# Kernel optimization log

Hardware: AMD Instinct MI355X
Metric: run time of the kernel (lower is better)

## Reference

```python
import jax, jax.numpy as jnp
import numpy as np

N_NODES = 50000
N_EDGES = 800000
IN_C, HID_C, OUT_C, HEADS = 128, 32, 64, 8
NEG_SLOPE = 0.2


def gat_layer(x, src, dst, W, a_src, a_dst, bias, concat, num_nodes):
    # W: [F_in, H*C]; a_src, a_dst: [H, C]; bias: [H*C] or [C]
    H, C = a_src.shape
    h = (x @ W).reshape(num_nodes, H, C)                      # [N,H,C]
    e_src = (h * a_src).sum(-1)                               # [N,H]
    e_dst = (h * a_dst).sum(-1)                               # [N,H]
    e = jax.nn.leaky_relu(e_src[src] + e_dst[dst], NEG_SLOPE) # [E,H]
    # segment softmax over incoming edges of each destination node
    m = jax.ops.segment_max(e, dst, num_segments=num_nodes)   # [N,H]
    ex = jnp.exp(e - m[dst])
    den = jax.ops.segment_sum(ex, dst, num_segments=num_nodes)
    alpha = ex / (den[dst] + 1e-16)                           # [E,H]
    out = jax.ops.segment_sum(h[src] * alpha[..., None], dst, num_segments=num_nodes)  # [N,H,C]
    out = out.reshape(num_nodes, H * C) if concat else out.mean(axis=1)
    return out + bias


def setup_inputs() -> dict:
    key = jax.random.key(0)
    ks = jax.random.split(key, 10)
    x = jax.random.normal(ks[0], (N_NODES, IN_C), dtype=jnp.float32)
    edge_index = jax.random.randint(ks[1], (2, N_EDGES), 0, N_NODES, dtype=jnp.int64)
    s1 = (2.0 / (IN_C + HID_C * HEADS)) ** 0.5
    s2 = (2.0 / (HID_C * HEADS + OUT_C)) ** 0.5
    return {
        "x": x,
        "edge_index": edge_index,
        "W1": jax.random.normal(ks[2], (IN_C, HEADS * HID_C), dtype=jnp.float32) * s1,
        "a_src1": jax.random.normal(ks[3], (HEADS, HID_C), dtype=jnp.float32) * 0.1,
        "a_dst1": jax.random.normal(ks[4], (HEADS, HID_C), dtype=jnp.float32) * 0.1,
        "b1": jnp.zeros((HEADS * HID_C,), dtype=jnp.float32),
        "W2": jax.random.normal(ks[5], (HEADS * HID_C, OUT_C), dtype=jnp.float32) * s2,
        "a_src2": jax.random.normal(ks[6], (1, OUT_C), dtype=jnp.float32) * 0.1,
        "a_dst2": jax.random.normal(ks[7], (1, OUT_C), dtype=jnp.float32) * 0.1,
        "b2": jnp.zeros((OUT_C,), dtype=jnp.float32),
    }


def reference(x, edge_index, W1, a_src1, a_dst1, b1, W2, a_src2, a_dst2, b2):
    # add self-loops (PyG GATConv default)
    loops = jnp.arange(N_NODES, dtype=edge_index.dtype)
    src = jnp.concatenate([edge_index[0], loops])
    dst = jnp.concatenate([edge_index[1], loops])
    # dropout layers are identity in eval mode
    h = gat_layer(x, src, dst, W1, a_src1, a_dst1, b1, True, N_NODES)
    h = jax.nn.elu(h)
    out = gat_layer(h, src, dst, W2, a_src2, a_dst2, b2, False, N_NODES)
    return out
```

## Files before the change

### kernel.cpp

```cpp
#include <hip/hip_runtime.h>
#include <math.h>

#define N_NODES 50000
#define N_EDGES 800000
#define E_TOT   850000
#define IN_C    128
#define HID_C   32
#define OUT_C   64
#define HEADS   8
#define F1      256
#define PAD     64
#define NDUMMY  1024
#define G1_BLOCKS 3125
#define CSR_BLOCKS 782

typedef __bf16 bf16x8 __attribute__((ext_vector_type(8)));
typedef float  f32x4  __attribute__((ext_vector_type(4)));
typedef float  f32x2  __attribute__((ext_vector_type(2)));
typedef unsigned short us8 __attribute__((ext_vector_type(8)));

__device__ __forceinline__ unsigned short f2b(float f) {
    unsigned u = __float_as_uint(f);
    u += 0x7FFF + ((u >> 16) & 1);
    return (unsigned short)(u >> 16);
}
__device__ __forceinline__ float b2f(unsigned short b) {
    return __uint_as_float(((unsigned)b) << 16);
}
__device__ __forceinline__ float blo(unsigned u) { return __uint_as_float(u << 16); }
__device__ __forceinline__ float bhi(unsigned u) { return __uint_as_float(u & 0xffff0000u); }
__device__ __forceinline__ f32x2 up2(unsigned u) {
    f32x2 r; r.x = blo(u); r.y = bhi(u); return r;
}

__global__ void convert_w(const float* __restrict__ W1, const float* __restrict__ W2,
                          const float* __restrict__ a_src2, const float* __restrict__ a_dst2,
                          unsigned short* __restrict__ W1t, unsigned short* __restrict__ W2t,
                          float* __restrict__ w2s, float* __restrict__ w2d,
                          int* __restrict__ deg, int* __restrict__ ssrc) {
    int gid = blockIdx.x * 256 + threadIdx.x;
    if (gid < N_NODES) {
        deg[gid] = 1;
        ssrc[gid * PAD] = gid;
    } else if (gid < N_NODES + NDUMMY) {
        deg[gid] = 0;
    }
    if (gid < 256) {
        float s = 0.f, dd = 0.f;
        for (int c = 0; c < OUT_C; c++) {
            float w = W2[gid * OUT_C + c];
            s  += w * a_src2[c];
            dd += w * a_dst2[c];
        }
        w2s[gid] = s; w2d[gid] = dd;
    }
    if (gid < 256 * 128) {
        int n = gid >> 7, k = gid & 127;
        W1t[gid] = f2b(W1[k * F1 + n]);
    } else if (gid < 256 * 128 + 64 * 256) {
        int o = gid - 256 * 128;
        int n = o >> 8, k = o & 255;
        W2t[o] = f2b(W2[k * OUT_C + n]);
    }
}

__global__ __launch_bounds__(256) void g1csr(const float* __restrict__ x,
                                             const unsigned short* __restrict__ W1t,
                                             const float* __restrict__ a_src,
                                             const float* __restrict__ a_dst,
                                             unsigned short* __restrict__ h1b,
                                             float* __restrict__ e_src,
                                             float* __restrict__ e_dst,
                                             const int* __restrict__ ei,
                                             int* __restrict__ deg,
                                             int* __restrict__ ssrc) {
    if (blockIdx.x >= G1_BLOCKS) {
        int e0 = (blockIdx.x - G1_BLOCKS) * 1024 + threadIdx.x;
        int s[4], d[4], p[4];
#pragma unroll
        for (int j = 0; j < 4; j++) {
            int e = e0 + j * 256;
            int le = (e < N_EDGES) ? e : (N_EDGES - 1);
            int es = ei[le];
            int ed = ei[N_EDGES + le];
            s[j] = es;
            d[j] = (e < N_EDGES) ? ed : (N_NODES + (e - N_EDGES));
        }
#pragma unroll
        for (int j = 0; j < 4; j++) p[j] = atomicAdd(&deg[d[j]], 1);
#pragma unroll
        for (int j = 0; j < 4; j++) ssrc[d[j] * PAD + p[j]] = s[j];
        return;
    }
    const int t = threadIdx.x;
    const int wave = t >> 6, lane = t & 63;
    const int mlane = lane & 15, quad = lane >> 4;
    const int row0 = blockIdx.x * 16;
    const int col0 = wave * 64;
    const float* xr = x + (size_t)(row0 + mlane) * IN_C;
    bf16x8 afr[4];
#pragma unroll
    for (int kc = 0; kc < 4; kc++) {
        float4 f0 = *(const float4*)&xr[kc * 32 + quad * 8];
        float4 f1 = *(const float4*)&xr[kc * 32 + quad * 8 + 4];
        us8 u;
        u[0] = f2b(f0.x); u[1] = f2b(f0.y); u[2] = f2b(f0.z); u[3] = f2b(f0.w);
        u[4] = f2b(f1.x); u[5] = f2b(f1.y); u[6] = f2b(f1.z); u[7] = f2b(f1.w);
        afr[kc] = __builtin_bit_cast(bf16x8, u);
    }
    f32x4 c[4];
#pragma unroll
    for (int nt = 0; nt < 4; nt++) c[nt] = (f32x4){0.f, 0.f, 0.f, 0.f};
#pragma unroll
    for (int kc = 0; kc < 4; kc++) {
#pragma unroll
        for (int nt = 0; nt < 4; nt++) {
            int col = col0 + nt * 16 + mlane;
            uint4 bw = *(const uint4*)&W1t[(size_t)col * IN_C + kc * 32 + quad * 8];
            bf16x8 b = __builtin_bit_cast(bf16x8, bw);
            c[nt] = __builtin_amdgcn_mfma_f32_16x16x32_bf16(afr[kc], b, c[nt], 0, 0, 0);
        }
    }
#pragma unroll
    for (int nt = 0; nt < 4; nt++) {
#pragma unroll
        for (int r = 0; r < 4; r++) {
            int gr = row0 + quad * 4 + r;
            h1b[(size_t)gr * F1 + col0 + nt * 16 + mlane] = f2b(c[nt][r]);
        }
    }
    float asA0 = a_src[col0 + mlane],      asA1 = a_src[col0 + 16 + mlane];
    float asB0 = a_src[col0 + 32 + mlane], asB1 = a_src[col0 + 48 + mlane];
    float adA0 = a_dst[col0 + mlane],      adA1 = a_dst[col0 + 16 + mlane];
    float adB0 = a_dst[col0 + 32 + mlane], adB1 = a_dst[col0 + 48 + mlane];
#pragma unroll
    for (int r = 0; r < 4; r++) {
        float psA = c[0][r] * asA0 + c[1][r] * asA1;
        float pdA = c[0][r] * adA0 + c[1][r] * adA1;
        float psB = c[2][r] * asB0 + c[3][r] * asB1;
        float pdB = c[2][r] * adB0 + c[3][r] * adB1;
#pragma unroll
        for (int off = 1; off < 16; off <<= 1) {
            psA += __shfl_xor(psA, off, 64);
            pdA += __shfl_xor(pdA, off, 64);
            psB += __shfl_xor(psB, off, 64);
            pdB += __shfl_xor(pdB, off, 64);
        }
        if (mlane == 0) {
            int gr = row0 + quad * 4 + r;
            e_src[gr * HEADS + wave * 2]     = psA;
            e_src[gr * HEADS + wave * 2 + 1] = psB;
            e_dst[gr * HEADS + wave * 2]     = pdA;
            e_dst[gr * HEADS + wave * 2 + 1] = pdB;
        }
    }
}

__global__ __launch_bounds__(256) void agg1s(const unsigned short* __restrict__ h1b,
                                             const float* __restrict__ e_src,
                                             const float* __restrict__ e_dst,
                                             const int* __restrict__ deg,
                                             const int* __restrict__ ssrc,
                                             const float* __restrict__ b1,
                                             const float* __restrict__ w2s,
                                             const float* __restrict__ w2d,
                                             unsigned short* __restrict__ hhb,
                                             float* __restrict__ e_src2,
                                             float* __restrict__ e_dst2) {
    int v = (blockIdx.x * 256 + threadIdx.x) >> 6;
    int lane = threadIdx.x & 63;
    int half = lane >> 5, l32 = lane & 31;
    int c0 = l32 * 8, h_acc = l32 >> 2;
    int c2 = c0 << 1;
    int h_exp = l32 & 7, j_exp = l32 >> 3;
    const char* h1c = (const char*)h1b;
    const char* esc = (const char*)e_src;
    int d = deg[v];
    int beg = v * PAD;
    int s_all = ssrc[beg + lane];
    float edh = e_dst[v * HEADS + h_exp];
    f32x2 acc[4];
#pragma unroll
    for (int k = 0; k < 4; k++) acc[k] = (f32x2){0.f, 0.f};
    float den = 0.f;
    int dm1 = d - 1;
    for (int k16 = 0; k16 < d; k16 += 16) {
        int slotA = k16 + half + 2 * j_exp;
        int slotB = slotA + 8;
        int sA = __shfl(s_all, (slotA < dm1 ? slotA : dm1), 64);
        int sB = __shfl(s_all, (slotB < dm1 ? slotB : dm1), 64);
        float eA = *(const float*)(esc + ((sA << 5) + (h_exp << 2))) + edh;
        float eB = *(const float*)(esc + ((sB << 5) + (h_exp << 2))) + edh;
        eA = fmaxf(eA, 0.2f * eA);
        eB = fmaxf(eB, 0.2f * eB);
        float wA = (slotA < d) ? __expf(eA) : 0.f;
        float wB = (slotB < d) ? __expf(eB) : 0.f;
        int s_j[8];
#pragma unroll
        for (int j = 0; j < 8; j++) {
            int slot = k16 + half + 2 * j;
            s_j[j] = __shfl(s_all, (slot < dm1 ? slot : dm1), 64);
        }
        float w_j[8];
#pragma unroll
        for (int j = 0; j < 4; j++) {
            w_j[j]     = __shfl(wA, (j << 3) | h_acc, 32);
            w_j[j + 4] = __shfl(wB, (j << 3) | h_acc, 32);
        }
        uint4 r[8];
#pragma unroll
        for (int j = 0; j < 8; j++)
            r[j] = *(const uint4*)(h1c + (((unsigned)s_j[j] << 9) + c2));
#pragma unroll
        for (int j = 0; j < 8; j++) {
            den += w_j[j];
            acc[0] += w_j[j] * up2(r[j].x);
            acc[1] += w_j[j] * up2(r[j].y);
            acc[2] += w_j[j] * up2(r[j].z);
            acc[3] += w_j[j] * up2(r[j].w);
        }
    }
    den += __shfl_xor(den, 32, 64);
#pragma unroll
    for (int k = 0; k < 4; k++) {
        acc[k].x += __shfl_xor(acc[k].x, 32, 64);
        acc[k].y += __shfl_xor(acc[k].y, 32, 64);
    }
    if (half == 0) {
        float dinv = 1.f / (den + 1e-16f);
        us8 o;
        float ps = 0.f, pd = 0.f;
#pragma unroll
        for (int k = 0; k < 4; k++) {
            float v0 = acc[k].x * dinv + b1[c0 + 2 * k];
            float v1 = acc[k].y * dinv + b1[c0 + 2 * k + 1];
            v0 = (v0 > 0.f) ? v0 : (__expf(v0) - 1.f);
            v1 = (v1 > 0.f) ? v1 : (__expf(v1) - 1.f);
            o[2 * k]     = f2b(v0);
            o[2 * k + 1] = f2b(v1);
            ps += v0 * w2s[c0 + 2 * k] + v1 * w2s[c0 + 2 * k + 1];
            pd += v0 * w2d[c0 + 2 * k] + v1 * w2d[c0 + 2 * k + 1];
        }
        *(us8*)&hhb[(size_t)v * F1 + c0] = o;
#pragma unroll
        for (int off = 1; off < 32; off <<= 1) {
            ps += __shfl_xor(ps, off, 32);
            pd += __shfl_xor(pd, off, 32);
        }
        if (l32 == 0) { e_src2[v] = ps; e_dst2[v] = pd; }
    }
}

__global__ __launch_bounds__(256) void gemm2_mfma(const unsigned short* __restrict__ hhb,
                                                  const unsigned short* __restrict__ W2t,
                                                  unsigned short* __restrict__ h2b) {
    __shared__ unsigned short A[16 * 264];
    const int t = threadIdx.x;
    const int wave = t >> 6, lane = t & 63;
    const int mlane = lane & 15, quad = lane >> 4;
    const int row0 = blockIdx.x * 16;
#pragma unroll
    for (int i = 0; i < 2; i++) {
        int u = t + i * 256;
        int row = u >> 5, seg = u & 31;
        uint4 w = *(const uint4*)&hhb[(size_t)(row0 + row) * F1 + seg * 8];
        *(uint4*)&A[row * 264 + seg * 8] = w;
    }
    __syncthreads();
    f32x4 cc = (f32x4){0.f, 0.f, 0.f, 0.f};
    const int col = wave * 16 + mlane;
#pragma unroll
    for (int kc = 0; kc < 8; kc++) {
        uint4 aw = *(const uint4*)&A[mlane * 264 + kc * 32 + quad * 8];
        bf16x8 a = __builtin_bit_cast(bf16x8, aw);
        uint4 bw = *(const uint4*)&W2t[(size_t)col * F1 + kc * 32 + quad * 8];
        bf16x8 b = __builtin_bit_cast(bf16x8, bw);
        cc = __builtin_amdgcn_mfma_f32_16x16x32_bf16(a, b, cc, 0, 0, 0);
    }
#pragma unroll
    for (int r = 0; r < 4; r++) {
        int gr = row0 + quad * 4 + r;
        h2b[(size_t)gr * OUT_C + wave * 16 + mlane] = f2b(cc[r]);
    }
}

__global__ __launch_bounds__(256) void agg2s(const unsigned short* __restrict__ h2b,
                                             const float* __restrict__ e_src,
                                             const float* __restrict__ e_dst,
                                             const int* __restrict__ deg,
                                             const int* __restrict__ ssrc,
                                             const float* __restrict__ b2,
                                             float* __restrict__ out) {
    int v = (blockIdx.x * 256 + threadIdx.x) >> 6;
    int lane = threadIdx.x & 63;
    int d = deg[v], beg = v * PAD, dm1 = d - 1;
    float ed = e_dst[v];
    int g = lane >> 3, l8 = lane & 7;
    int c0 = l8 * 8;
    int c2 = c0 << 1;
    const char* h2c = (const char*)h2b;
    const char* esc = (const char*)e_src;
    int s_raw = ssrc[beg + lane];
    int s_cl = s_raw < 0 ? 0 : (s_raw > N_NODES - 1 ? N_NODES - 1 : s_raw);
    float e_own = *(const float*)(esc + (s_cl << 2)) + ed;
    e_own = fmaxf(e_own, 0.2f * e_own);
    float w_own = (lane < d) ? __expf(e_own) : 0.f;
    f32x2 acc[4];
#pragma unroll
    for (int k = 0; k < 4; k++) acc[k] = (f32x2){0.f, 0.f};
    float den = 0.f;
    for (int k16 = 0; k16 < d; k16 += 16) {
        int slot0 = k16 + g, slot1 = slot0 + 8;
        int t0 = slot0 < dm1 ? slot0 : dm1;
        int t1 = slot1 < dm1 ? slot1 : dm1;
        int s0 = __shfl(s_cl, t0, 64);
        int s1 = __shfl(s_cl, t1, 64);
        float w0 = __shfl(w_own, t0, 64); w0 = (slot0 < d) ? w0 : 0.f;
        float w1 = __shfl(w_own, t1, 64); w1 = (slot1 < d) ? w1 : 0.f;
        den += w0 + w1;
        uint4 r0 = *(const uint4*)(h2c + ((s0 << 7) + c2));
        uint4 r1 = *(const uint4*)(h2c + ((s1 << 7) + c2));
        acc[0] += w0 * up2(r0.x) + w1 * up2(r1.x);
        acc[1] += w0 * up2(r0.y) + w1 * up2(r1.y);
        acc[2] += w0 * up2(r0.z) + w1 * up2(r1.z);
        acc[3] += w0 * up2(r0.w) + w1 * up2(r1.w);
    }
    den += __shfl_xor(den, 8, 64);
    den += __shfl_xor(den, 16, 64);
    den += __shfl_xor(den, 32, 64);
#pragma unroll
    for (int k = 0; k < 4; k++) {
        acc[k].x += __shfl_xor(acc[k].x, 8, 64);
        acc[k].y += __shfl_xor(acc[k].y, 8, 64);
        acc[k].x += __shfl_xor(acc[k].x, 16, 64);
        acc[k].y += __shfl_xor(acc[k].y, 16, 64);
        acc[k].x += __shfl_xor(acc[k].x, 32, 64);
        acc[k].y += __shfl_xor(acc[k].y, 32, 64);
    }
    if (g == 0) {
        float dinv = 1.f / (den + 1e-16f);
        float4 lo, hi;
        lo.x = acc[0].x * dinv + b2[c0 + 0]; lo.y = acc[0].y * dinv + b2[c0 + 1];
        lo.z = acc[1].x * dinv + b2[c0 + 2]; lo.w = acc[1].y * dinv + b2[c0 + 3];
        hi.x = acc[2].x * dinv + b2[c0 + 4]; hi.y = acc[2].y * dinv + b2[c0 + 5];
        hi.z = acc[3].x * dinv + b2[c0 + 6]; hi.w = acc[3].y * dinv + b2[c0 + 7];
        *(float4*)&out[(size_t)v * OUT_C + c0] = lo;
        *(float4*)&out[(size_t)v * OUT_C + c0 + 4] = hi;
    }
}

extern "C" void kernel_launch(void* const* d_in, const int* in_sizes, int n_in,
                              void* d_out, int out_size, void* d_ws, size_t ws_size,
                              hipStream_t stream) {
    const float* x      = (const float*)d_in[0];
    const int*   ei     = (const int*)d_in[1];
    const float* W1     = (const float*)d_in[2];
    const float* a_src1 = (const float*)d_in[3];
    const float* a_dst1 = (const float*)d_in[4];
    const float* b1     = (const float*)d_in[5];
    const float* W2     = (const float*)d_in[6];
    const float* a_src2 = (const float*)d_in[7];
    const float* a_dst2 = (const float*)d_in[8];
    const float* b2     = (const float*)d_in[9];
    float* out = (float*)d_out;

    char* ws = (char*)d_ws;
    size_t off = 0;
    auto alloc = [&](size_t bytes) { void* p = ws + off; off = (off + bytes + 255) & ~(size_t)255; return p; };
    unsigned short* h1b = (unsigned short*)alloc((size_t)N_NODES * F1 * 2);
    unsigned short* hhb = (unsigned short*)alloc((size_t)N_NODES * F1 * 2);
    unsigned short* h2b = (unsigned short*)alloc((size_t)N_NODES * OUT_C * 2);
    unsigned short* W1t = (unsigned short*)alloc((size_t)256 * 128 * 2);
    unsigned short* W2t = (unsigned short*)alloc((size_t)64 * 256 * 2);
    float* w2s    = (float*)alloc((size_t)256 * 4);
    float* w2d    = (float*)alloc((size_t)256 * 4);
    float* e_src1 = (float*)alloc((size_t)N_NODES * HEADS * 4);
    float* e_dst1 = (float*)alloc((size_t)N_NODES * HEADS * 4);
    float* e_src2 = (float*)alloc((size_t)N_NODES * 4);
    float* e_dst2 = (float*)alloc((size_t)N_NODES * 4);
    int*   deg    = (int*)alloc((size_t)(N_NODES + NDUMMY) * 4);
    int*   ssrc   = (int*)alloc((size_t)(N_NODES + NDUMMY) * PAD * 4);
    (void)ws_size; (void)n_in; (void)in_sizes; (void)out_size;

    const int node_waves = (N_NODES + 3) / 4;

    convert_w<<<200, 256, 0, stream>>>(W1, W2, a_src2, a_dst2, W1t, W2t, w2s, w2d, deg, ssrc);
    g1csr<<<G1_BLOCKS + CSR_BLOCKS, 256, 0, stream>>>(x, W1t, a_src1, a_dst1,
                                                      h1b, e_src1, e_dst1, ei, deg, ssrc);
    agg1s<<<node_waves, 256, 0, stream>>>(h1b, e_src1, e_dst1, deg, ssrc, b1,
                                          w2s, w2d, hhb, e_src2, e_dst2);
    gemm2_mfma<<<G1_BLOCKS, 256, 0, stream>>>(hhb, W2t, h2b);
    agg2s<<<node_waves, 256, 0, stream>>>(h2b, e_src2, e_dst2, deg, ssrc, b2, out);
}
```

Baseline: 283.9 us.

## Pad degree counters to 64 bytes and move CSR build blocks first

Degree counters are now spaced 16 ints apart, so each node's atomic counter sits on its own 64-byte segment and concurrent atomics on neighbouring nodes stop contending on one cache line. The CSR-building blocks now come first in the fused launch and use one edge per thread instead of four, so the scatter work is scheduled ahead of the GEMM tiles. The dummy-node padding is removed because 3125*256 is exactly the edge count. In exchange the deg array grows 16x, and its reads in the aggregation kernels become strided rather than contiguous.

```diff
diff --git a/kernel.cpp b/kernel.cpp
--- a/kernel.cpp
+++ b/kernel.cpp
@@ -10,9 +10,8 @@
 #define HEADS   8
 #define F1      256
 #define PAD     64
-#define NDUMMY  1024
 #define G1_BLOCKS 3125
-#define CSR_BLOCKS 782
+#define CSR_BLOCKS 3125
 
 typedef __bf16 bf16x8 __attribute__((ext_vector_type(8)));
 typedef float  f32x4  __attribute__((ext_vector_type(4)));
@@ -40,10 +39,8 @@
                           int* __restrict__ deg, int* __restrict__ ssrc) {
     int gid = blockIdx.x * 256 + threadIdx.x;
     if (gid < N_NODES) {
-        deg[gid] = 1;
+        deg[gid << 4] = 1;
         ssrc[gid * PAD] = gid;
-    } else if (gid < N_NODES + NDUMMY) {
-        deg[gid] = 0;
     }
     if (gid < 256) {
         float s = 0.f, dd = 0.f;
@@ -74,28 +71,18 @@
                                              const int* __restrict__ ei,
                                              int* __restrict__ deg,
                                              int* __restrict__ ssrc) {
-    if (blockIdx.x >= G1_BLOCKS) {
-        int e0 = (blockIdx.x - G1_BLOCKS) * 1024 + threadIdx.x;
-        int s[4], d[4], p[4];
-#pragma unroll
-        for (int j = 0; j < 4; j++) {
-            int e = e0 + j * 256;
-            int le = (e < N_EDGES) ? e : (N_EDGES - 1);
-            int es = ei[le];
-            int ed = ei[N_EDGES + le];
-            s[j] = es;
-            d[j] = (e < N_EDGES) ? ed : (N_NODES + (e - N_EDGES));
-        }
-#pragma unroll
-        for (int j = 0; j < 4; j++) p[j] = atomicAdd(&deg[d[j]], 1);
-#pragma unroll
-        for (int j = 0; j < 4; j++) ssrc[d[j] * PAD + p[j]] = s[j];
+    if (blockIdx.x < CSR_BLOCKS) {
+        int e = blockIdx.x * 256 + threadIdx.x;
+        int s  = ei[e];
+        int dv = ei[N_EDGES + e];
+        int p = atomicAdd(&deg[dv << 4], 1);
+        ssrc[dv * PAD + p] = s;
         return;
     }
     const int t = threadIdx.x;
     const int wave = t >> 6, lane = t & 63;
     const int mlane = lane & 15, quad = lane >> 4;
-    const int row0 = blockIdx.x * 16;
+    const int row0 = (blockIdx.x - CSR_BLOCKS) * 16;
     const int col0 = wave * 64;
     const float* xr = x + (size_t)(row0 + mlane) * IN_C;
     bf16x8 afr[4];
@@ -175,7 +162,7 @@
     int h_exp = l32 & 7, j_exp = l32 >> 3;
     const char* h1c = (const char*)h1b;
     const char* esc = (const char*)e_src;
-    int d = deg[v];
+    int d = deg[v << 4];
     int beg = v * PAD;
     int s_all = ssrc[beg + lane];
     float edh = e_dst[v * HEADS + h_exp];
@@ -293,7 +280,7 @@
                                              float* __restrict__ out) {
     int v = (blockIdx.x * 256 + threadIdx.x) >> 6;
     int lane = threadIdx.x & 63;
-    int d = deg[v], beg = v * PAD, dm1 = d - 1;
+    int d = deg[v << 4], beg = v * PAD, dm1 = d - 1;
     float ed = e_dst[v];
     int g = lane >> 3, l8 = lane & 7;
     int c0 = l8 * 8;
@@ -378,14 +365,14 @@
     float* e_dst1 = (float*)alloc((size_t)N_NODES * HEADS * 4);
     float* e_src2 = (float*)alloc((size_t)N_NODES * 4);
     float* e_dst2 = (float*)alloc((size_t)N_NODES * 4);
-    int*   deg    = (int*)alloc((size_t)(N_NODES + NDUMMY) * 4);
-    int*   ssrc   = (int*)alloc((size_t)(N_NODES + NDUMMY) * PAD * 4);
+    int*   deg    = (int*)alloc((size_t)N_NODES * 16 * 4);
+    int*   ssrc   = (int*)alloc((size_t)N_NODES * PAD * 4);
     (void)ws_size; (void)n_in; (void)in_sizes; (void)out_size;
 
     const int node_waves = (N_NODES + 3) / 4;
 
     convert_w<<<200, 256, 0, stream>>>(W1, W2, a_src2, a_dst2, W1t, W2t, w2s, w2d, deg, ssrc);
-    g1csr<<<G1_BLOCKS + CSR_BLOCKS, 256, 0, stream>>>(x, W1t, a_src1, a_dst1,
+    g1csr<<<CSR_BLOCKS + G1_BLOCKS, 256, 0, stream>>>(x, W1t, a_src1, a_dst1,
                                                       h1b, e_src1, e_dst1, ei, deg, ssrc);
     agg1s<<<node_waves, 256, 0, stream>>>(h1b, e_src1, e_dst1, deg, ssrc, b1,
                                           w2s, w2d, hhb, e_src2, e_dst2);
```

Measured after the change: 297.4 us. 1.05x slower.
